# Performance work log

Measured on AMD Instinct MI355X. Metric: run time of the kernel, lower is better.

## Reference

```python
import jax, jax.numpy as jnp
import numpy as np

NBACTIONS = 4
TOTALNBINPUTS = 17  # RFSIZE*RFSIZE + ADDINPUT + NBACTIONS = 9 + 4 + 4
H = 4096


def setup_inputs() -> dict:
    key = jax.random.key(0)
    ks = jax.random.split(key, 12)
    x = jax.random.normal(ks[0], (1, TOTALNBINPUTS), dtype=jnp.float32)
    hidden = 0.1 * jax.random.normal(ks[1], (1, H), dtype=jnp.float32)
    hebb = 0.01 * jax.random.normal(ks[2], (H, H), dtype=jnp.float32)
    # i2h Linear(17 -> H); store weight as [in, out]
    Wi = jax.random.normal(ks[3], (TOTALNBINPUTS, H), dtype=jnp.float32) / np.sqrt(TOTALNBINPUTS)
    bi = jax.random.normal(ks[4], (H,), dtype=jnp.float32) * 0.01
    # plastic recurrent params (0.01 * rand, as in torch init)
    w = 0.01 * jax.random.uniform(ks[5], (H, H), dtype=jnp.float32)
    alpha = 0.01 * jax.random.uniform(ks[6], (H, H), dtype=jnp.float32)
    eta = jnp.full((1,), 0.01, dtype=jnp.float32)
    # heads
    Wo = jax.random.normal(ks[7], (H, NBACTIONS), dtype=jnp.float32) / np.sqrt(H)
    bo = jax.random.normal(ks[8], (NBACTIONS,), dtype=jnp.float32) * 0.01
    Wv = jax.random.normal(ks[9], (H, 1), dtype=jnp.float32) / np.sqrt(H)
    bv = jax.random.normal(ks[10], (1,), dtype=jnp.float32) * 0.01
    return {"x": x, "hidden": hidden, "hebb": hebb, "Wi": Wi, "bi": bi,
            "w": w, "alpha": alpha, "eta": eta, "Wo": Wo, "bo": bo,
            "Wv": Wv, "bv": bv}


def reference(x, hidden, hebb, Wi, bi, w, alpha, eta, Wo, bo, Wv, bv):
    # type='plastic', rule='hebb', activ='tanh'
    # hactiv = tanh(i2h(x) + hidden @ (w + alpha * hebb))   [1, H]
    hactiv = jnp.tanh(x @ Wi + bi + hidden @ (w + alpha * hebb))
    # hebb <- (1 - eta) * hebb + eta * outer(hidden, hactiv)   [H, H]
    hebb_new = (1.0 - eta) * hebb + eta * jnp.outer(hidden[0], hactiv[0])
    activout = jax.nn.softmax(hactiv @ Wo + bo, axis=-1)  # [1, NBACTIONS]
    valueout = hactiv @ Wv + bv                            # [1, 1]
    return (activout, valueout, hactiv, hebb_new)
```

## Files before the change

kernel.cpp:

```cpp
#include <hip/hip_runtime.h>
#include <math.h>

#define H 4096
#define NIN 17
#define H4 (H / 4)
#define NSPLIT 512
#define ROWS_PER_SPLIT (H / NSPLIT)
#define NSPLIT2 32
#define KC_BLOCKS (H * (H / 1024))

typedef float vf4 __attribute__((ext_vector_type(4)));

#define OUT_HACTIV_OFF  5
#define OUT_HEBB_OFF    4101
#define OUT_PARTIAL_OFF 4104
#define OUT_PARTIAL2_OFF (OUT_PARTIAL_OFF + NSPLIT * H)

__global__ __launch_bounds__(256, 2) void kA(const float* __restrict__ hidden,
                                             const float* __restrict__ w,
                                             const float* __restrict__ alpha,
                                             const float* __restrict__ hebb,
                                             float* __restrict__ partial) {
    const int t = threadIdx.x;
    const int b = blockIdx.x;
    const int r0 = b * ROWS_PER_SPLIT;
    const vf4* __restrict__ w4 = (const vf4*)w;
    const vf4* __restrict__ a4 = (const vf4*)alpha;
    const vf4* __restrict__ b4 = (const vf4*)hebb;

    vf4 acc[4];
#pragma unroll
    for (int k = 0; k < 4; ++k) acc[k] = (vf4)(0.f);

#pragma unroll 2
    for (int r = 0; r < ROWS_PER_SPLIT; ++r) {
        const int i = r0 + r;
        const float hv = hidden[i];
        const int rowbase = i * H4;
#pragma unroll
        for (int k = 0; k < 4; ++k) {
            const int idx = rowbase + t + k * 256;
            const vf4 wv = __builtin_nontemporal_load(&w4[idx]);
            const vf4 av = __builtin_nontemporal_load(&a4[idx]);
            const vf4 bv = b4[idx];
            acc[k] += hv * (wv + av * bv);
        }
    }
    vf4* __restrict__ p4 = (vf4*)partial;
#pragma unroll
    for (int k = 0; k < 4; ++k)
        p4[(b << 10) + t + k * 256] = acc[k];
}

__global__ __launch_bounds__(256) void kB1(const float* __restrict__ partial,
                                           float* __restrict__ partial2) {
    const int j4 = blockIdx.x * 256 + threadIdx.x;
    const vf4* __restrict__ p4 = (const vf4*)partial;
    vf4 acc = (vf4)(0.f);
#pragma unroll
    for (int s = 0; s < NSPLIT / NSPLIT2; ++s) {
        acc += p4[(blockIdx.y * (NSPLIT / NSPLIT2) + s) * H4 + j4];
    }
    ((vf4*)partial2)[blockIdx.y * H4 + j4] = acc;
}

__global__ __launch_bounds__(256) void kB2(const float* __restrict__ x,
                                           const float* __restrict__ Wi,
                                           const float* __restrict__ bi,
                                           const float* __restrict__ partial2,
                                           float* __restrict__ hactiv) {
    const int j = blockIdx.x * 256 + threadIdx.x;
    float s = bi[j];
#pragma unroll
    for (int k = 0; k < NIN; ++k) s += x[k] * Wi[k * H + j];
#pragma unroll
    for (int sp = 0; sp < NSPLIT2; ++sp) s += partial2[sp * H + j];
    hactiv[j] = tanhf(s);
}

__global__ __launch_bounds__(256) void kC(const float* __restrict__ hebb,
                                          const float* __restrict__ hidden,
                                          const float* __restrict__ eta_p,
                                          const float* __restrict__ Wo,
                                          const float* __restrict__ bo,
                                          const float* __restrict__ Wv,
                                          const float* __restrict__ bv,
                                          float* __restrict__ out) {
    const float* __restrict__ hactiv = out + OUT_HACTIV_OFF;
    float* __restrict__ hebb_out = out + OUT_HEBB_OFF;

    if (blockIdx.x < (unsigned)KC_BLOCKS) {
        const unsigned base = blockIdx.x * 1024u;
        const unsigned i = base >> 12;
        const float eta = eta_p[0];
        const float em = 1.f - eta;
        const float eh = eta * hidden[i];
#pragma unroll
        for (int k = 0; k < 4; ++k) {
            const unsigned g = base + (unsigned)(k * 256) + threadIdx.x;
            const unsigned col = g & (H - 1);
            const float hb = hebb[g];
            const float v = em * hb + eh * hactiv[col];
            __builtin_nontemporal_store(v, &hebb_out[g]);
        }
    } else {
        __shared__ float red[5][256];
        float a0 = 0.f, a1 = 0.f, a2 = 0.f, a3 = 0.f, av = 0.f;
        const vf4* __restrict__ Wo4 = (const vf4*)Wo;
        for (int i = threadIdx.x; i < H; i += 256) {
            const float h = hactiv[i];
            const vf4 wo = Wo4[i];
            a0 += h * wo.x;
            a1 += h * wo.y;
            a2 += h * wo.z;
            a3 += h * wo.w;
            av += h * Wv[i];
        }
        red[0][threadIdx.x] = a0;
        red[1][threadIdx.x] = a1;
        red[2][threadIdx.x] = a2;
        red[3][threadIdx.x] = a3;
        red[4][threadIdx.x] = av;
        __syncthreads();
        for (int s = 128; s > 0; s >>= 1) {
            if ((int)threadIdx.x < s) {
#pragma unroll
                for (int k = 0; k < 5; ++k)
                    red[k][threadIdx.x] += red[k][threadIdx.x + s];
            }
            __syncthreads();
        }
        if (threadIdx.x == 0) {
            const float z0 = red[0][0] + bo[0];
            const float z1 = red[1][0] + bo[1];
            const float z2 = red[2][0] + bo[2];
            const float z3 = red[3][0] + bo[3];
            const float m = fmaxf(fmaxf(z0, z1), fmaxf(z2, z3));
            const float e0 = expf(z0 - m);
            const float e1 = expf(z1 - m);
            const float e2 = expf(z2 - m);
            const float e3 = expf(z3 - m);
            const float inv = 1.f / (e0 + e1 + e2 + e3);
            out[0] = e0 * inv;
            out[1] = e1 * inv;
            out[2] = e2 * inv;
            out[3] = e3 * inv;
            out[4] = red[4][0] + bv[0];
        }
    }
}

extern "C" void kernel_launch(void* const* d_in, const int* in_sizes, int n_in,
                              void* d_out, int out_size, void* d_ws, size_t ws_size,
                              hipStream_t stream) {
    const float* x      = (const float*)d_in[0];
    const float* hidden = (const float*)d_in[1];
    const float* hebb   = (const float*)d_in[2];
    const float* Wi     = (const float*)d_in[3];
    const float* bi     = (const float*)d_in[4];
    const float* w      = (const float*)d_in[5];
    const float* alpha  = (const float*)d_in[6];
    const float* eta    = (const float*)d_in[7];
    const float* Wo     = (const float*)d_in[8];
    const float* bo     = (const float*)d_in[9];
    const float* Wv     = (const float*)d_in[10];
    const float* bv     = (const float*)d_in[11];
    float* out = (float*)d_out;

    float* partial  = out + OUT_PARTIAL_OFF;
    float* partial2 = out + OUT_PARTIAL2_OFF;
    float* hactiv   = out + OUT_HACTIV_OFF;

    kA<<<NSPLIT, 256, 0, stream>>>(hidden, w, alpha, hebb, partial);
    kB1<<<dim3(4, NSPLIT2), 256, 0, stream>>>(partial, partial2);
    kB2<<<16, 256, 0, stream>>>(x, Wi, bi, partial2, hactiv);
    kC<<<KC_BLOCKS + 1, 256, 0, stream>>>(hebb, hidden, eta, Wo, bo, Wv, bv, out);
}
```

Baseline: 254.2 us.

## Split matvec blocks across columns and give each hebb-update block a full row

kA now launches a 2D grid of 4 column chunks by 512 row splits, and each thread accumulates one vf4 column over 8 rows instead of four vf4 columns. This raises block count and occupancy, and the nontemporal loads and the two-block-per-CU launch bound are dropped. kC now processes one full 4096-element row per block with 16 iterations, cutting the block count fourfold and simplifying index math. The aim is better latency hiding on the bandwidth-bound passes, at the cost of changed cache behaviour for w and alpha streams.

```diff
diff --git a/kernel.cpp b/kernel.cpp
--- a/kernel.cpp
+++ b/kernel.cpp
@@ -7,7 +7,6 @@
 #define NSPLIT 512
 #define ROWS_PER_SPLIT (H / NSPLIT)
 #define NSPLIT2 32
-#define KC_BLOCKS (H * (H / 1024))
 
 typedef float vf4 __attribute__((ext_vector_type(4)));
 
@@ -16,40 +15,29 @@
 #define OUT_PARTIAL_OFF 4104
 #define OUT_PARTIAL2_OFF (OUT_PARTIAL_OFF + NSPLIT * H)
 
-__global__ __launch_bounds__(256, 2) void kA(const float* __restrict__ hidden,
-                                             const float* __restrict__ w,
-                                             const float* __restrict__ alpha,
-                                             const float* __restrict__ hebb,
-                                             float* __restrict__ partial) {
+__global__ __launch_bounds__(256) void kA(const float* __restrict__ hidden,
+                                          const float* __restrict__ w,
+                                          const float* __restrict__ alpha,
+                                          const float* __restrict__ hebb,
+                                          float* __restrict__ partial) {
     const int t = threadIdx.x;
-    const int b = blockIdx.x;
+    const int cx = blockIdx.x;
+    const int b = blockIdx.y;
+    const int col4 = cx * 256 + t;
     const int r0 = b * ROWS_PER_SPLIT;
     const vf4* __restrict__ w4 = (const vf4*)w;
     const vf4* __restrict__ a4 = (const vf4*)alpha;
     const vf4* __restrict__ b4 = (const vf4*)hebb;
 
-    vf4 acc[4];
-#pragma unroll
-    for (int k = 0; k < 4; ++k) acc[k] = (vf4)(0.f);
-
-#pragma unroll 2
+    vf4 acc = (vf4)(0.f);
+#pragma unroll 4
     for (int r = 0; r < ROWS_PER_SPLIT; ++r) {
         const int i = r0 + r;
         const float hv = hidden[i];
-        const int rowbase = i * H4;
-#pragma unroll
-        for (int k = 0; k < 4; ++k) {
-            const int idx = rowbase + t + k * 256;
-            const vf4 wv = __builtin_nontemporal_load(&w4[idx]);
-            const vf4 av = __builtin_nontemporal_load(&a4[idx]);
-            const vf4 bv = b4[idx];
-            acc[k] += hv * (wv + av * bv);
-        }
+        const int idx = i * H4 + col4;
+        acc += hv * (w4[idx] + a4[idx] * b4[idx]);
     }
-    vf4* __restrict__ p4 = (vf4*)partial;
-#pragma unroll
-    for (int k = 0; k < 4; ++k)
-        p4[(b << 10) + t + k * 256] = acc[k];
+    ((vf4*)partial)[b * H4 + col4] = acc;
 }
 
 __global__ __launch_bounds__(256) void kB1(const float* __restrict__ partial,
@@ -89,19 +77,18 @@
     const float* __restrict__ hactiv = out + OUT_HACTIV_OFF;
     float* __restrict__ hebb_out = out + OUT_HEBB_OFF;
 
-    if (blockIdx.x < (unsigned)KC_BLOCKS) {
-        const unsigned base = blockIdx.x * 1024u;
-        const unsigned i = base >> 12;
+    if (blockIdx.x < (unsigned)H) {
+        const unsigned i = blockIdx.x;
+        const unsigned base = i << 12;
         const float eta = eta_p[0];
         const float em = 1.f - eta;
         const float eh = eta * hidden[i];
 #pragma unroll
-        for (int k = 0; k < 4; ++k) {
-            const unsigned g = base + (unsigned)(k * 256) + threadIdx.x;
-            const unsigned col = g & (H - 1);
-            const float hb = hebb[g];
-            const float v = em * hb + eh * hactiv[col];
-            __builtin_nontemporal_store(v, &hebb_out[g]);
+        for (int k = 0; k < 16; ++k) {
+            const unsigned c = (unsigned)(k * 256) + threadIdx.x;
+            const float hb = hebb[base + c];
+            const float v = em * hb + eh * hactiv[c];
+            __builtin_nontemporal_store(v, &hebb_out[base + c]);
         }
     } else {
         __shared__ float red[5][256];
@@ -171,8 +158,8 @@
     float* partial2 = out + OUT_PARTIAL2_OFF;
     float* hactiv   = out + OUT_HACTIV_OFF;
 
-    kA<<<NSPLIT, 256, 0, stream>>>(hidden, w, alpha, hebb, partial);
+    kA<<<dim3(4, NSPLIT), 256, 0, stream>>>(hidden, w, alpha, hebb, partial);
     kB1<<<dim3(4, NSPLIT2), 256, 0, stream>>>(partial, partial2);
     kB2<<<16, 256, 0, stream>>>(x, Wi, bi, partial2, hactiv);
-    kC<<<KC_BLOCKS + 1, 256, 0, stream>>>(hebb, hidden, eta, Wo, bo, Wv, bv, out);
+    kC<<<H + 1, 256, 0, stream>>>(hebb, hidden, eta, Wo, bo, Wv, bv, out);
 }
```

New measurement: 267.6 us. 5.3% more time.

## Merge two-stage partial reduction into one kernel and vectorize hebb update loads

Applied to the files above, without the earlier changes.

Replaces the two reduction kernels (kB1, kB2) with a single kernel in which four thread groups each sum 128 split partials per column, combine them through shared memory, then add the input projection and apply tanh. This removes one launch and the intermediate partial2 buffer. The hebb update kernel now runs 512-thread blocks that each cover two rows, reading hebb as float4 but writing scalar nontemporal stores, which cuts the block count. The new reduction runs only 64 blocks with scalar column reads, so the 8 MB partial read may be less parallel than before.

```diff
diff --git a/kernel.cpp b/kernel.cpp
--- a/kernel.cpp
+++ b/kernel.cpp
@@ -6,15 +6,12 @@
 #define H4 (H / 4)
 #define NSPLIT 512
 #define ROWS_PER_SPLIT (H / NSPLIT)
-#define NSPLIT2 32
-#define KC_BLOCKS (H * (H / 1024))
 
 typedef float vf4 __attribute__((ext_vector_type(4)));
 
 #define OUT_HACTIV_OFF  5
 #define OUT_HEBB_OFF    4101
 #define OUT_PARTIAL_OFF 4104
-#define OUT_PARTIAL2_OFF (OUT_PARTIAL_OFF + NSPLIT * H)
 
 __global__ __launch_bounds__(256, 2) void kA(const float* __restrict__ hidden,
                                              const float* __restrict__ w,
@@ -52,33 +49,31 @@
         p4[(b << 10) + t + k * 256] = acc[k];
 }
 
-__global__ __launch_bounds__(256) void kB1(const float* __restrict__ partial,
-                                           float* __restrict__ partial2) {
-    const int j4 = blockIdx.x * 256 + threadIdx.x;
-    const vf4* __restrict__ p4 = (const vf4*)partial;
-    vf4 acc = (vf4)(0.f);
+__global__ __launch_bounds__(256) void kB(const float* __restrict__ x,
+                                          const float* __restrict__ Wi,
+                                          const float* __restrict__ bi,
+                                          const float* __restrict__ partial,
+                                          float* __restrict__ hactiv) {
+    const int t = threadIdx.x;
+    const int j = blockIdx.x * 64 + (t & 63);
+    const int sq = t >> 6;
+    float acc = 0.f;
+#pragma unroll 8
+    for (int s = sq * 128; s < sq * 128 + 128; ++s)
+        acc += partial[s * H + j];
+
+    __shared__ float red[4][64];
+    red[sq][t & 63] = acc;
+    __syncthreads();
+    if (t < 64) {
+        float s = red[0][t] + red[1][t] + red[2][t] + red[3][t] + bi[j];
 #pragma unroll
-    for (int s = 0; s < NSPLIT / NSPLIT2; ++s) {
-        acc += p4[(blockIdx.y * (NSPLIT / NSPLIT2) + s) * H4 + j4];
+        for (int k = 0; k < NIN; ++k) s += x[k] * Wi[k * H + j];
+        hactiv[j] = tanhf(s);
     }
-    ((vf4*)partial2)[blockIdx.y * H4 + j4] = acc;
 }
 
-__global__ __launch_bounds__(256) void kB2(const float* __restrict__ x,
-                                           const float* __restrict__ Wi,
-                                           const float* __restrict__ bi,
-                                           const float* __restrict__ partial2,
-                                           float* __restrict__ hactiv) {
-    const int j = blockIdx.x * 256 + threadIdx.x;
-    float s = bi[j];
-#pragma unroll
-    for (int k = 0; k < NIN; ++k) s += x[k] * Wi[k * H + j];
-#pragma unroll
-    for (int sp = 0; sp < NSPLIT2; ++sp) s += partial2[sp * H + j];
-    hactiv[j] = tanhf(s);
-}
-
-__global__ __launch_bounds__(256) void kC(const float* __restrict__ hebb,
+__global__ __launch_bounds__(512) void kC(const float* __restrict__ hebb,
                                           const float* __restrict__ hidden,
                                           const float* __restrict__ eta_p,
                                           const float* __restrict__ Wo,
@@ -88,26 +83,42 @@
                                           float* __restrict__ out) {
     const float* __restrict__ hactiv = out + OUT_HACTIV_OFF;
     float* __restrict__ hebb_out = out + OUT_HEBB_OFF;
+    const int t = threadIdx.x;
 
-    if (blockIdx.x < (unsigned)KC_BLOCKS) {
-        const unsigned base = blockIdx.x * 1024u;
-        const unsigned i = base >> 12;
+    if (blockIdx.x < (unsigned)(H / 2)) {
+        const unsigned b = blockIdx.x;
         const float eta = eta_p[0];
         const float em = 1.f - eta;
-        const float eh = eta * hidden[i];
+        const float eh0 = eta * hidden[2 * b];
+        const float eh1 = eta * hidden[2 * b + 1];
+        const vf4* __restrict__ hb4 = (const vf4*)hebb;
+
+        vf4 hb[4];
+        unsigned g4[4];
 #pragma unroll
         for (int k = 0; k < 4; ++k) {
-            const unsigned g = base + (unsigned)(k * 256) + threadIdx.x;
-            const unsigned col = g & (H - 1);
-            const float hb = hebb[g];
-            const float v = em * hb + eh * hactiv[col];
-            __builtin_nontemporal_store(v, &hebb_out[g]);
+            g4[k] = b * 2048u + (unsigned)(k * 512) + t;
+            hb[k] = hb4[g4[k]];
+        }
+#pragma unroll
+        for (int k = 0; k < 4; ++k) {
+            const unsigned col4 = g4[k] & 1023u;
+            const float eh = (k < 2) ? eh0 : eh1;
+            const float ha0 = hactiv[col4 * 4 + 0];
+            const float ha1 = hactiv[col4 * 4 + 1];
+            const float ha2 = hactiv[col4 * 4 + 2];
+            const float ha3 = hactiv[col4 * 4 + 3];
+            const unsigned e = g4[k] * 4u;
+            __builtin_nontemporal_store(em * hb[k].x + eh * ha0, &hebb_out[e + 0]);
+            __builtin_nontemporal_store(em * hb[k].y + eh * ha1, &hebb_out[e + 1]);
+            __builtin_nontemporal_store(em * hb[k].z + eh * ha2, &hebb_out[e + 2]);
+            __builtin_nontemporal_store(em * hb[k].w + eh * ha3, &hebb_out[e + 3]);
         }
     } else {
-        __shared__ float red[5][256];
+        __shared__ float red[5][512];
         float a0 = 0.f, a1 = 0.f, a2 = 0.f, a3 = 0.f, av = 0.f;
         const vf4* __restrict__ Wo4 = (const vf4*)Wo;
-        for (int i = threadIdx.x; i < H; i += 256) {
+        for (int i = t; i < H; i += 512) {
             const float h = hactiv[i];
             const vf4 wo = Wo4[i];
             a0 += h * wo.x;
@@ -116,21 +127,21 @@
             a3 += h * wo.w;
             av += h * Wv[i];
         }
-        red[0][threadIdx.x] = a0;
-        red[1][threadIdx.x] = a1;
-        red[2][threadIdx.x] = a2;
-        red[3][threadIdx.x] = a3;
-        red[4][threadIdx.x] = av;
+        red[0][t] = a0;
+        red[1][t] = a1;
+        red[2][t] = a2;
+        red[3][t] = a3;
+        red[4][t] = av;
         __syncthreads();
-        for (int s = 128; s > 0; s >>= 1) {
-            if ((int)threadIdx.x < s) {
+        for (int s = 256; s > 0; s >>= 1) {
+            if (t < s) {
 #pragma unroll
                 for (int k = 0; k < 5; ++k)
-                    red[k][threadIdx.x] += red[k][threadIdx.x + s];
+                    red[k][t] += red[k][t + s];
             }
             __syncthreads();
         }
-        if (threadIdx.x == 0) {
+        if (t == 0) {
             const float z0 = red[0][0] + bo[0];
             const float z1 = red[1][0] + bo[1];
             const float z2 = red[2][0] + bo[2];
@@ -167,12 +178,10 @@
     const float* bv     = (const float*)d_in[11];
     float* out = (float*)d_out;
 
-    float* partial  = out + OUT_PARTIAL_OFF;
-    float* partial2 = out + OUT_PARTIAL2_OFF;
-    float* hactiv   = out + OUT_HACTIV_OFF;
+    float* partial = out + OUT_PARTIAL_OFF;
+    float* hactiv  = out + OUT_HACTIV_OFF;
 
     kA<<<NSPLIT, 256, 0, stream>>>(hidden, w, alpha, hebb, partial);
-    kB1<<<dim3(4, NSPLIT2), 256, 0, stream>>>(partial, partial2);
-    kB2<<<16, 256, 0, stream>>>(x, Wi, bi, partial2, hactiv);
-    kC<<<KC_BLOCKS + 1, 256, 0, stream>>>(hebb, hidden, eta, Wo, bo, Wv, bv, out);
+    kB<<<64, 256, 0, stream>>>(x, Wi, bi, partial, hactiv);
+    kC<<<H / 2 + 1, 512, 0, stream>>>(hebb, hidden, eta, Wo, bo, Wv, bv, out);
 }
```

New measurement: 255.4 us. Within noise of the previous version (+0.5%).
